# Kernel optimization log

Measured on AMD Instinct MI355X. Metric: run time of the kernel, lower is better.

## Reference

```python
import jax, jax.numpy as jnp
import numpy as np

NUM_EMBEDDINGS = 2048
EMBEDDING_DIM = 64
COMMITMENT_COST = 0.25


def setup_inputs() -> dict:
    key = jax.random.key(0)
    k1, k2 = jax.random.split(key)
    inputs = jax.random.normal(k1, (64, 32, 32, EMBEDDING_DIM), dtype=jnp.float32)
    # lecun_uniform-style scale on fan_in = embedding_dim
    limit = np.sqrt(3.0 / EMBEDDING_DIM).astype(np.float32)
    codebook = jax.random.uniform(k2, (EMBEDDING_DIM, NUM_EMBEDDINGS), dtype=jnp.float32,
                                  minval=-limit, maxval=limit)
    return {"inputs": inputs, "codebook": codebook}


def reference(inputs, codebook):
    lax = jax.lax
    flat = jnp.reshape(inputs, (-1, EMBEDDING_DIM))          # [N, D]
    # squared Euclidean distances to each code: [N, K]
    distances = (jnp.sum(jnp.square(flat), 1, keepdims=True)
                 - 2.0 * jnp.matmul(flat, codebook)
                 + jnp.sum(jnp.square(codebook), 0, keepdims=True))
    encoding_indices = jnp.argmin(distances, 1)              # [N]
    flat_q = jnp.take(codebook, encoding_indices, axis=1).swapaxes(1, 0)  # [N, D]
    quantized = jnp.reshape(flat_q, inputs.shape)

    codebook_loss = jnp.mean(jnp.square(quantized - lax.stop_gradient(inputs)))
    commitment_loss = COMMITMENT_COST * jnp.mean(
        jnp.square(lax.stop_gradient(quantized) - inputs))

    encodings = jax.nn.one_hot(encoding_indices, NUM_EMBEDDINGS, dtype=jnp.float32)
    avg_probs = jnp.mean(encodings, 0)
    perplexity = jnp.exp(-jnp.sum(avg_probs * jnp.log(avg_probs + 1e-10)))

    ste = inputs + lax.stop_gradient(quantized - inputs)
    return (ste, perplexity, codebook_loss, commitment_loss)
```

## Files before the change

### kernel.cpp

```cpp
#include <hip/hip_runtime.h>
#include <math.h>

#define KCODES 2048
#define DIM 64
#define NROWS 65536
#define NELEM (NROWS * DIM)

#define WS_HIST 0
#define WS_C2   8192
#define WS_C2S  16384
#define WS_SSE  24576
#define WS_P    32768

#define EPS_PK 33

typedef float  floatx4 __attribute__((ext_vector_type(4)));
typedef short  short8  __attribute__((ext_vector_type(8)));

__device__ __forceinline__ unsigned short f2bf(float f) {
  union { float f; unsigned u; } a; a.f = f;
  unsigned r = (a.u + 0x7FFFu + ((a.u >> 16) & 1u)) >> 16;
  return (unsigned short)r;
}
__device__ __forceinline__ float bf2f(unsigned short h) {
  union { unsigned u; float f; } a; a.u = ((unsigned)h) << 16;
  return a.f;
}

__global__ void vq_colnorm(const float* __restrict__ cb, float* __restrict__ c2,
                           float* __restrict__ c2s) {
  int k = blockIdx.x * 256 + threadIdx.x;
  float s = 0.f;
#pragma unroll
  for (int d = 0; d < DIM; ++d) {
    float v = cb[d * KCODES + k];
    s = fmaf(v, v, s);
  }
  c2[k] = s;
  c2s[k] = (s + 64.0f) * 16384.0f;
}

__global__ void vq_prep(const float* __restrict__ cb, char* __restrict__ P) {
  int tid = blockIdx.x * 256 + threadIdx.x;
  int code = tid & (KCODES - 1);
  int g = tid >> 11;
  short8 hh, ll;
#pragma unroll
  for (int e = 0; e < 8; ++e) {
    float v = -2.0f * cb[(size_t)(g * 8 + e) * KCODES + code];
    unsigned short hb = f2bf(v);
    float lo = v - bf2f(hb);
    hh[e] = (short)hb;
    ll[e] = (short)f2bf(lo);
  }
  int tile = code >> 5;
  int sn = code & 31;
  int pb = g ^ (sn & 7);
  size_t base = (size_t)tile * 8192 + sn * 128 + pb * 16;
  *(short8*)(P + base) = hh;
  *(short8*)(P + base + 4096) = ll;
}

__device__ __forceinline__ void stage_tile(const char* P, char* lds,
                                           int tile, int w, int lane) {
  const char* gp = P + (size_t)tile * 8192 + w * 1024 + lane * 16;
  char* lp = lds + w * 1024 + lane * 16;
  __builtin_amdgcn_global_load_lds(
      (const __attribute__((address_space(1))) unsigned*)gp,
      (__attribute__((address_space(3))) unsigned*)lp, 16, 0, 0);
  __builtin_amdgcn_global_load_lds(
      (const __attribute__((address_space(1))) unsigned*)(gp + 4096),
      (__attribute__((address_space(3))) unsigned*)(lp + 4096), 16, 0, 0);
}

__global__ __launch_bounds__(256, 2) void vq_main(
    const float* __restrict__ inp, const float* __restrict__ cb,
    const float* __restrict__ c2, const float* __restrict__ c2s,
    const char* __restrict__ P, int* __restrict__ hist,
    float* __restrict__ sse, float* __restrict__ out)
{
  __shared__ __align__(16) char Bstage[2][8192];
  __shared__ float s_c2s[KCODES];
  __shared__ int   s_k[128];
  __shared__ int   s_nflag;
  __shared__ int   s_frows[128];
  __shared__ float s_rd[256];
  __shared__ int   s_rk[256];
  __shared__ float s_red[4];

  const int t    = threadIdx.x;
  const int lane = t & 63;
  const int wave = __builtin_amdgcn_readfirstlane(t >> 6);
  const int c    = lane & 15;
  const int q    = lane >> 4;
  const int c7   = c & 7;
  const int rowbase = blockIdx.x * 128 + wave * 32;

  if (t == 0) s_nflag = 0;

#pragma unroll
  for (int i = 0; i < KCODES / 256; ++i) s_c2s[i * 256 + t] = c2s[i * 256 + t];

  short8 Ah[2][2], Al[2][2];
#pragma unroll
  for (int r = 0; r < 2; ++r) {
#pragma unroll
    for (int s = 0; s < 2; ++s) {
      const float* px = inp + (size_t)(rowbase + r * 16 + c) * 64 + s * 32 + q * 8;
      float4 u0 = *(const float4*)px;
      float4 u1 = *(const float4*)(px + 4);
      float u[8] = {u0.x, u0.y, u0.z, u0.w, u1.x, u1.y, u1.z, u1.w};
      short8 hh, ll;
#pragma unroll
      for (int e = 0; e < 8; ++e) {
        float xs = u[e] * 16384.0f;
        unsigned short hb = f2bf(xs);
        float lo = xs - bf2f(hb);
        hh[e] = (short)hb;
        ll[e] = (short)f2bf(lo);
      }
      Ah[r][s] = hh; Al[r][s] = ll;
    }
  }

  unsigned d1[8], d2[8];
#pragma unroll
  for (int i = 0; i < 8; ++i) { d1[i] = 0xFFFFFFFFu; d2[i] = 0xFFFFFFFFu; }

  stage_tile(P, Bstage[0], 0, wave, lane);
  __syncthreads();

  const floatx4 zero = {0.f, 0.f, 0.f, 0.f};

#pragma unroll 2
  for (int j = 0; j < 64; ++j) {
    const int buf = j & 1;
    if (j + 1 < 64) stage_tile(P, Bstage[1 - buf], j + 1, wave, lane);

    float c2v0 = s_c2s[j * 32 + c];
    float c2v1 = s_c2s[j * 32 + 16 + c];

#pragma unroll
    for (int nt = 0; nt < 2; ++nt) {
      const int rowi = nt * 16 + c;
      const char* bp = &Bstage[buf][rowi * 128];
      short8 bh0 = *(const short8*)(bp + ((0 + q) ^ c7) * 16);
      short8 bh1 = *(const short8*)(bp + ((4 + q) ^ c7) * 16);
      short8 bl0 = *(const short8*)(bp + 4096 + ((0 + q) ^ c7) * 16);
      short8 bl1 = *(const short8*)(bp + 4096 + ((4 + q) ^ c7) * 16);
      const float c2v = nt ? c2v1 : c2v0;
      const unsigned kcn = j * 32 + nt * 16 + c;
#pragma unroll
      for (int r = 0; r < 2; ++r) {
        floatx4 acc = __builtin_amdgcn_mfma_f32_16x16x32_bf16(Al[r][1], bh1, zero, 0, 0, 0);
        acc = __builtin_amdgcn_mfma_f32_16x16x32_bf16(Ah[r][1], bl1, acc, 0, 0, 0);
        acc = __builtin_amdgcn_mfma_f32_16x16x32_bf16(Al[r][0], bh0, acc, 0, 0, 0);
        acc = __builtin_amdgcn_mfma_f32_16x16x32_bf16(Ah[r][0], bl0, acc, 0, 0, 0);
        acc = __builtin_amdgcn_mfma_f32_16x16x32_bf16(Ah[r][1], bh1, acc, 0, 0, 0);
        acc = __builtin_amdgcn_mfma_f32_16x16x32_bf16(Ah[r][0], bh0, acc, 0, 0, 0);
#pragma unroll
        for (int reg = 0; reg < 4; ++reg) {
          float dds = acc[reg] + c2v;
          unsigned u = (((unsigned)dds) << 11) + kcn;
          const int i = r * 4 + reg;
          d2[i] = min(d2[i], max(d1[i], u));
          d1[i] = min(d1[i], u);
        }
      }
    }
    __syncthreads();
  }

#pragma unroll
  for (int i = 0; i < 8; ++i) {
    unsigned D1 = d1[i], D2 = d2[i];
#pragma unroll
    for (int off = 1; off < 16; off <<= 1) {
      unsigned o1 = (unsigned)__shfl_xor((int)D1, off, 64);
      unsigned o2 = (unsigned)__shfl_xor((int)D2, off, 64);
      D2 = min(min(D2, o2), max(D1, o1));
      D1 = min(D1, o1);
    }
    if (c == 0) {
      int lrow = wave * 32 + (i >> 2) * 16 + q * 4 + (i & 3);
      s_k[lrow] = (int)(D1 & 2047u);
      if ((int)((D2 >> 11) - (D1 >> 11)) < EPS_PK) {
        int idx = atomicAdd(&s_nflag, 1);
        s_frows[idx] = lrow;
      }
    }
  }
  __syncthreads();

  const int nf = s_nflag;
  for (int f = 0; f < nf; ++f) {
    const int lrow = s_frows[f];
    const float* xr = inp + (size_t)(blockIdx.x * 128 + lrow) * 64;
    float xs[64];
    float x2 = 0.f;
#pragma unroll
    for (int i = 0; i < 16; ++i) {
      float4 v = *(const float4*)(xr + i * 4);
      xs[4 * i + 0] = v.x; xs[4 * i + 1] = v.y; xs[4 * i + 2] = v.z; xs[4 * i + 3] = v.w;
      x2 = fmaf(v.x, v.x, x2); x2 = fmaf(v.y, v.y, x2);
      x2 = fmaf(v.z, v.z, x2); x2 = fmaf(v.w, v.w, x2);
    }
    float dot[8];
#pragma unroll
    for (int cc = 0; cc < 8; ++cc) dot[cc] = 0.f;
    const float* cp = cb + t * 8;
#pragma unroll 4
    for (int d = 0; d < 64; ++d) {
      float xd = xs[d];
#pragma unroll
      for (int cc = 0; cc < 8; ++cc)
        dot[cc] = fmaf(xd, cp[(size_t)d * KCODES + cc], dot[cc]);
    }
    float bd = INFINITY; int bk = 0;
#pragma unroll
    for (int cc = 0; cc < 8; ++cc) {
      float dd = (x2 - 2.0f * dot[cc]) + c2[t * 8 + cc];
      if (dd < bd) { bd = dd; bk = t * 8 + cc; }
    }
    s_rd[t] = bd; s_rk[t] = bk;
    __syncthreads();
    for (int s = 128; s >= 1; s >>= 1) {
      if (t < s) {
        if (s_rd[t + s] < s_rd[t]) { s_rd[t] = s_rd[t + s]; s_rk[t] = s_rk[t + s]; }
      }
      __syncthreads();
    }
    if (t == 0) s_k[lrow] = s_rk[0];
    __syncthreads();
  }

  if (t < 128) atomicAdd(&hist[s_k[t]], 1);

  const int fr = t >> 1;
  const int fd = (t & 1) * 32;
  const int grow = blockIdx.x * 128 + fr;
  const int myk = s_k[fr];
  const float* xrow = inp + (size_t)grow * 64 + fd;
  float* orow = out + (size_t)grow * 64 + fd;
  float serr = 0.f;
#pragma unroll
  for (int i = 0; i < 32; ++i) {
    float xv = xrow[i];
    float qv = cb[(size_t)(fd + i) * KCODES + myk];
    float dq = qv - xv;
    serr = fmaf(dq, dq, serr);
    orow[i] = xv + dq;
  }
#pragma unroll
  for (int off = 32; off > 0; off >>= 1) serr += __shfl_down(serr, off, 64);
  if (lane == 0) s_red[wave] = serr;
  __syncthreads();
  if (t == 0) atomicAdd(sse, s_red[0] + s_red[1] + s_red[2] + s_red[3]);
}

__global__ void vq_final(const int* __restrict__ hist,
                         const float* __restrict__ sse,
                         float* __restrict__ out) {
  __shared__ float s_red[4];
  const int t = threadIdx.x;
  float s = 0.f;
  for (int k = t; k < KCODES; k += 256) {
    float p = (float)hist[k] * (1.0f / NROWS);
    s += p * logf(p + 1e-10f);
  }
#pragma unroll
  for (int off = 32; off > 0; off >>= 1) s += __shfl_down(s, off, 64);
  if ((t & 63) == 0) s_red[t >> 6] = s;
  __syncthreads();
  if (t == 0) {
    float tot = s_red[0] + s_red[1] + s_red[2] + s_red[3];
    out[NELEM] = expf(-tot);
    float cl = *sse * (1.0f / NELEM);
    out[NELEM + 1] = cl;
    out[NELEM + 2] = 0.25f * cl;
  }
}

extern "C" void kernel_launch(void* const* d_in, const int* in_sizes, int n_in,
                              void* d_out, int out_size, void* d_ws, size_t ws_size,
                              hipStream_t stream) {
  const float* inp = (const float*)d_in[0];
  const float* cb  = (const float*)d_in[1];
  float* out = (float*)d_out;
  char* ws = (char*)d_ws;
  int*   hist = (int*)(ws + WS_HIST);
  float* c2   = (float*)(ws + WS_C2);
  float* c2s  = (float*)(ws + WS_C2S);
  float* sse  = (float*)(ws + WS_SSE);
  char*  P    = ws + WS_P;

  hipMemsetAsync(d_ws, 0, WS_SSE + 16, stream);
  vq_colnorm<<<KCODES / 256, 256, 0, stream>>>(cb, c2, c2s);
  vq_prep<<<KCODES * 8 / 256, 256, 0, stream>>>(cb, P);
  vq_main<<<NROWS / 128, 256, 0, stream>>>(inp, cb, c2, c2s, P, hist, sse, out);
  vq_final<<<1, 256, 0, stream>>>(hist, sse, out);
}
```

Before: 187.8 us.

## Restructure VQ kernel: register-resident codebook tiles, split codes across waves, fused launches

```diff
diff --git a/kernel.cpp b/kernel.cpp
--- a/kernel.cpp
+++ b/kernel.cpp
@@ -10,6 +10,7 @@
 #define WS_C2   8192
 #define WS_C2S  16384
 #define WS_SSE  24576
+#define WS_DONE 24580
 #define WS_P    32768
 
 #define EPS_PK 33
@@ -26,87 +27,77 @@
   union { unsigned u; float f; } a; a.u = ((unsigned)h) << 16;
   return a.f;
 }
-
-__global__ void vq_colnorm(const float* __restrict__ cb, float* __restrict__ c2,
-                           float* __restrict__ c2s) {
-  int k = blockIdx.x * 256 + threadIdx.x;
-  float s = 0.f;
-#pragma unroll
-  for (int d = 0; d < DIM; ++d) {
-    float v = cb[d * KCODES + k];
-    s = fmaf(v, v, s);
-  }
-  c2[k] = s;
-  c2s[k] = (s + 64.0f) * 16384.0f;
-}
-
-__global__ void vq_prep(const float* __restrict__ cb, char* __restrict__ P) {
-  int tid = blockIdx.x * 256 + threadIdx.x;
-  int code = tid & (KCODES - 1);
-  int g = tid >> 11;
-  short8 hh, ll;
+__device__ __forceinline__ unsigned umin2(unsigned a, unsigned b) { return a < b ? a : b; }
+__device__ __forceinline__ unsigned umax2(unsigned a, unsigned b) { return a > b ? a : b; }
+
+__global__ void vq_prep(const float* __restrict__ cb, char* __restrict__ P,
+                        float* __restrict__ c2, float* __restrict__ c2s,
+                        int* __restrict__ hist, float* __restrict__ sse,
+                        int* __restrict__ done) {
+  const int id = blockIdx.x * 256 + threadIdx.x;
+  const int c   = id & 15;
+  const int q   = (id >> 4) & 3;
+  const int s   = (id >> 6) & 1;
+  const int p   = (id >> 7) & 1;
+  const int t16 = id >> 8;
+  const int code = t16 * 16 + c;
+  const int d0 = s * 32 + q * 8;
+  short8 o;
 #pragma unroll
   for (int e = 0; e < 8; ++e) {
-    float v = -2.0f * cb[(size_t)(g * 8 + e) * KCODES + code];
+    float v = -2.0f * cb[(size_t)(d0 + e) * KCODES + code];
     unsigned short hb = f2bf(v);
     float lo = v - bf2f(hb);
-    hh[e] = (short)hb;
-    ll[e] = (short)f2bf(lo);
-  }
-  int tile = code >> 5;
-  int sn = code & 31;
-  int pb = g ^ (sn & 7);
-  size_t base = (size_t)tile * 8192 + sn * 128 + pb * 16;
-  *(short8*)(P + base) = hh;
-  *(short8*)(P + base + 4096) = ll;
-}
-
-__device__ __forceinline__ void stage_tile(const char* P, char* lds,
-                                           int tile, int w, int lane) {
-  const char* gp = P + (size_t)tile * 8192 + w * 1024 + lane * 16;
-  char* lp = lds + w * 1024 + lane * 16;
-  __builtin_amdgcn_global_load_lds(
-      (const __attribute__((address_space(1))) unsigned*)gp,
-      (__attribute__((address_space(3))) unsigned*)lp, 16, 0, 0);
-  __builtin_amdgcn_global_load_lds(
-      (const __attribute__((address_space(1))) unsigned*)(gp + 4096),
-      (__attribute__((address_space(3))) unsigned*)(lp + 4096), 16, 0, 0);
+    o[e] = p ? (short)f2bf(lo) : (short)hb;
+  }
+  *(short8*)(P + (size_t)id * 16) = o;
+
+  if (id < KCODES) {
+    float ss = 0.f;
+#pragma unroll
+    for (int d = 0; d < DIM; ++d) {
+      float v = cb[d * KCODES + id];
+      ss = fmaf(v, v, ss);
+    }
+    c2[id] = ss;
+    c2s[id] = (ss + 64.0f) * 16384.0f;
+    hist[id] = 0;
+    if (id == 0) { *sse = 0.f; *done = 0; }
+  }
 }
 
 __global__ __launch_bounds__(256, 2) void vq_main(
     const float* __restrict__ inp, const float* __restrict__ cb,
     const float* __restrict__ c2, const float* __restrict__ c2s,
     const char* __restrict__ P, int* __restrict__ hist,
-    float* __restrict__ sse, float* __restrict__ out)
+    float* __restrict__ sse, int* __restrict__ done, float* __restrict__ out)
 {
-  __shared__ __align__(16) char Bstage[2][8192];
-  __shared__ float s_c2s[KCODES];
+  __shared__ unsigned s_m1[2][128], s_m2[2][128];
   __shared__ int   s_k[128];
   __shared__ int   s_nflag;
   __shared__ int   s_frows[128];
   __shared__ float s_rd[256];
   __shared__ int   s_rk[256];
   __shared__ float s_red[4];
+  __shared__ int   s_last;
 
   const int t    = threadIdx.x;
   const int lane = t & 63;
   const int wave = __builtin_amdgcn_readfirstlane(t >> 6);
+  const int rg   = wave & 1;
+  const int ch   = wave >> 1;
   const int c    = lane & 15;
   const int q    = lane >> 4;
-  const int c7   = c & 7;
-  const int rowbase = blockIdx.x * 128 + wave * 32;
+  const int rowbase = blockIdx.x * 128 + rg * 64;
 
   if (t == 0) s_nflag = 0;
 
-#pragma unroll
-  for (int i = 0; i < KCODES / 256; ++i) s_c2s[i * 256 + t] = c2s[i * 256 + t];
-
-  short8 Ah[2][2], Al[2][2];
-#pragma unroll
-  for (int r = 0; r < 2; ++r) {
+  short8 Ah[4][2], Al[4][2];
+#pragma unroll
+  for (int rt = 0; rt < 4; ++rt) {
 #pragma unroll
     for (int s = 0; s < 2; ++s) {
-      const float* px = inp + (size_t)(rowbase + r * 16 + c) * 64 + s * 32 + q * 8;
+      const float* px = inp + (size_t)(rowbase + rt * 16 + c) * 64 + s * 32 + q * 8;
       float4 u0 = *(const float4*)px;
       float4 u1 = *(const float4*)(px + 4);
       float u[8] = {u0.x, u0.y, u0.z, u0.w, u1.x, u1.y, u1.z, u1.w};
@@ -119,75 +110,99 @@
         hh[e] = (short)hb;
         ll[e] = (short)f2bf(lo);
       }
-      Ah[r][s] = hh; Al[r][s] = ll;
-    }
-  }
-
-  unsigned d1[8], d2[8];
-#pragma unroll
-  for (int i = 0; i < 8; ++i) { d1[i] = 0xFFFFFFFFu; d2[i] = 0xFFFFFFFFu; }
-
-  stage_tile(P, Bstage[0], 0, wave, lane);
-  __syncthreads();
-
-  const floatx4 zero = {0.f, 0.f, 0.f, 0.f};
-
-#pragma unroll 2
-  for (int j = 0; j < 64; ++j) {
-    const int buf = j & 1;
-    if (j + 1 < 64) stage_tile(P, Bstage[1 - buf], j + 1, wave, lane);
-
-    float c2v0 = s_c2s[j * 32 + c];
-    float c2v1 = s_c2s[j * 32 + 16 + c];
-
+      Ah[rt][s] = hh; Al[rt][s] = ll;
+    }
+  }
+
+  unsigned d1[16], d2[16];
+#pragma unroll
+  for (int i = 0; i < 16; ++i) { d1[i] = 0xFFFFFFFFu; d2[i] = 0xFFFFFFFFu; }
+
+  const char* Pw = P + ((size_t)ch << 18);
+  const float* c2sw = c2s + ch * 1024;
+
+  auto load_tile = [&](short8 B[2][4], int j) {
+#pragma unroll
+    for (int nt = 0; nt < 2; ++nt)
+#pragma unroll
+      for (int f = 0; f < 4; ++f)
+        B[nt][f] = *(const short8*)(Pw + ((((j * 2 + nt) * 4 + f) << 10) + lane * 16));
+  };
+
+  auto comp_tile = [&](short8 B[2][4], int j) {
 #pragma unroll
     for (int nt = 0; nt < 2; ++nt) {
-      const int rowi = nt * 16 + c;
-      const char* bp = &Bstage[buf][rowi * 128];
-      short8 bh0 = *(const short8*)(bp + ((0 + q) ^ c7) * 16);
-      short8 bh1 = *(const short8*)(bp + ((4 + q) ^ c7) * 16);
-      short8 bl0 = *(const short8*)(bp + 4096 + ((0 + q) ^ c7) * 16);
-      short8 bl1 = *(const short8*)(bp + 4096 + ((4 + q) ^ c7) * 16);
-      const float c2v = nt ? c2v1 : c2v0;
-      const unsigned kcn = j * 32 + nt * 16 + c;
-#pragma unroll
-      for (int r = 0; r < 2; ++r) {
-        floatx4 acc = __builtin_amdgcn_mfma_f32_16x16x32_bf16(Al[r][1], bh1, zero, 0, 0, 0);
-        acc = __builtin_amdgcn_mfma_f32_16x16x32_bf16(Ah[r][1], bl1, acc, 0, 0, 0);
-        acc = __builtin_amdgcn_mfma_f32_16x16x32_bf16(Al[r][0], bh0, acc, 0, 0, 0);
-        acc = __builtin_amdgcn_mfma_f32_16x16x32_bf16(Ah[r][0], bl0, acc, 0, 0, 0);
-        acc = __builtin_amdgcn_mfma_f32_16x16x32_bf16(Ah[r][1], bh1, acc, 0, 0, 0);
-        acc = __builtin_amdgcn_mfma_f32_16x16x32_bf16(Ah[r][0], bh0, acc, 0, 0, 0);
+      float c2v = c2sw[j * 32 + nt * 16 + c];
+      floatx4 ci = {c2v, c2v, c2v, c2v};
+      floatx4 acc[4];
+#pragma unroll
+      for (int rt = 0; rt < 4; ++rt)
+        acc[rt] = __builtin_amdgcn_mfma_f32_16x16x32_bf16(Al[rt][1], B[nt][1], ci, 0, 0, 0);
+#pragma unroll
+      for (int rt = 0; rt < 4; ++rt)
+        acc[rt] = __builtin_amdgcn_mfma_f32_16x16x32_bf16(Ah[rt][1], B[nt][3], acc[rt], 0, 0, 0);
+#pragma unroll
+      for (int rt = 0; rt < 4; ++rt)
+        acc[rt] = __builtin_amdgcn_mfma_f32_16x16x32_bf16(Al[rt][0], B[nt][0], acc[rt], 0, 0, 0);
+#pragma unroll
+      for (int rt = 0; rt < 4; ++rt)
+        acc[rt] = __builtin_amdgcn_mfma_f32_16x16x32_bf16(Ah[rt][0], B[nt][2], acc[rt], 0, 0, 0);
+#pragma unroll
+      for (int rt = 0; rt < 4; ++rt)
+        acc[rt] = __builtin_amdgcn_mfma_f32_16x16x32_bf16(Ah[rt][1], B[nt][1], acc[rt], 0, 0, 0);
+#pragma unroll
+      for (int rt = 0; rt < 4; ++rt)
+        acc[rt] = __builtin_amdgcn_mfma_f32_16x16x32_bf16(Ah[rt][0], B[nt][0], acc[rt], 0, 0, 0);
+      const unsigned kcn = ch * 1024 + j * 32 + nt * 16 + c;
+#pragma unroll
+      for (int rt = 0; rt < 4; ++rt)
 #pragma unroll
         for (int reg = 0; reg < 4; ++reg) {
-          float dds = acc[reg] + c2v;
-          unsigned u = (((unsigned)dds) << 11) + kcn;
-          const int i = r * 4 + reg;
-          d2[i] = min(d2[i], max(d1[i], u));
-          d1[i] = min(d1[i], u);
+          unsigned u = (((unsigned)acc[rt][reg]) << 11) + kcn;
+          const int i = rt * 4 + reg;
+          d2[i] = umin2(d2[i], umax2(d1[i], u));
+          d1[i] = umin2(d1[i], u);
         }
-      }
-    }
-    __syncthreads();
-  }
-
-#pragma unroll
-  for (int i = 0; i < 8; ++i) {
+    }
+  };
+
+  short8 BA[2][4], BB[2][4];
+  load_tile(BA, 0);
+#pragma unroll 1
+  for (int j = 0; j < 32; j += 2) {
+    load_tile(BB, j + 1);
+    comp_tile(BA, j);
+    if (j + 2 < 32) load_tile(BA, j + 2);
+    comp_tile(BB, j + 1);
+  }
+
+#pragma unroll
+  for (int i = 0; i < 16; ++i) {
     unsigned D1 = d1[i], D2 = d2[i];
 #pragma unroll
     for (int off = 1; off < 16; off <<= 1) {
       unsigned o1 = (unsigned)__shfl_xor((int)D1, off, 64);
       unsigned o2 = (unsigned)__shfl_xor((int)D2, off, 64);
-      D2 = min(min(D2, o2), max(D1, o1));
-      D1 = min(D1, o1);
+      D2 = umin2(umin2(D2, o2), umax2(D1, o1));
+      D1 = umin2(D1, o1);
     }
     if (c == 0) {
-      int lrow = wave * 32 + (i >> 2) * 16 + q * 4 + (i & 3);
-      s_k[lrow] = (int)(D1 & 2047u);
-      if ((int)((D2 >> 11) - (D1 >> 11)) < EPS_PK) {
-        int idx = atomicAdd(&s_nflag, 1);
-        s_frows[idx] = lrow;
-      }
+      int lr = rg * 64 + (i >> 2) * 16 + q * 4 + (i & 3);
+      s_m1[ch][lr] = D1;
+      s_m2[ch][lr] = D2;
+    }
+  }
+  __syncthreads();
+
+  if (t < 128) {
+    unsigned a1 = s_m1[0][t], a2 = s_m2[0][t];
+    unsigned b1 = s_m1[1][t], b2 = s_m2[1][t];
+    unsigned D1 = umin2(a1, b1);
+    unsigned D2 = umin2(umin2(a2, b2), umax2(a1, b1));
+    s_k[t] = (int)(D1 & 2047u);
+    if ((int)((D2 >> 11) - (D1 >> 11)) < EPS_PK) {
+      int idx = atomicAdd(&s_nflag, 1);
+      s_frows[idx] = t;
     }
   }
   __syncthreads();
@@ -256,28 +271,28 @@
   if (lane == 0) s_red[wave] = serr;
   __syncthreads();
   if (t == 0) atomicAdd(sse, s_red[0] + s_red[1] + s_red[2] + s_red[3]);
-}
-
-__global__ void vq_final(const int* __restrict__ hist,
-                         const float* __restrict__ sse,
-                         float* __restrict__ out) {
-  __shared__ float s_red[4];
-  const int t = threadIdx.x;
-  float s = 0.f;
-  for (int k = t; k < KCODES; k += 256) {
-    float p = (float)hist[k] * (1.0f / NROWS);
-    s += p * logf(p + 1e-10f);
-  }
-#pragma unroll
-  for (int off = 32; off > 0; off >>= 1) s += __shfl_down(s, off, 64);
-  if ((t & 63) == 0) s_red[t >> 6] = s;
+
+  __threadfence();
+  if (t == 0) s_last = (atomicAdd(done, 1) == (int)gridDim.x - 1);
   __syncthreads();
-  if (t == 0) {
-    float tot = s_red[0] + s_red[1] + s_red[2] + s_red[3];
-    out[NELEM] = expf(-tot);
-    float cl = *sse * (1.0f / NELEM);
-    out[NELEM + 1] = cl;
-    out[NELEM + 2] = 0.25f * cl;
+  if (s_last) {
+    float s = 0.f;
+    for (int k = t; k < KCODES; k += 256) {
+      int h = atomicAdd(&hist[k], 0);
+      float pp = (float)h * (1.0f / NROWS);
+      s += pp * logf(pp + 1e-10f);
+    }
+#pragma unroll
+    for (int off = 32; off > 0; off >>= 1) s += __shfl_down(s, off, 64);
+    if (lane == 0) s_red[wave] = s;
+    __syncthreads();
+    if (t == 0) {
+      float tot = s_red[0] + s_red[1] + s_red[2] + s_red[3];
+      out[NELEM] = expf(-tot);
+      float cl = atomicAdd(sse, 0.0f) * (1.0f / NELEM);
+      out[NELEM + 1] = cl;
+      out[NELEM + 2] = 0.25f * cl;
+    }
   }
 }
 
@@ -292,11 +307,9 @@
   float* c2   = (float*)(ws + WS_C2);
   float* c2s  = (float*)(ws + WS_C2S);
   float* sse  = (float*)(ws + WS_SSE);
+  int*   done = (int*)(ws + WS_DONE);
   char*  P    = ws + WS_P;
 
-  hipMemsetAsync(d_ws, 0, WS_SSE + 16, stream);
-  vq_colnorm<<<KCODES / 256, 256, 0, stream>>>(cb, c2, c2s);
-  vq_prep<<<KCODES * 8 / 256, 256, 0, stream>>>(cb, P);
-  vq_main<<<NROWS / 128, 256, 0, stream>>>(inp, cb, c2, c2s, P, hist, sse, out);
-  vq_final<<<1, 256, 0, stream>>>(hist, sse, out);
-}
+  vq_prep<<<128, 256, 0, stream>>>(cb, P, c2, c2s, hist, sse, done);
+  vq_main<<<NROWS / 128, 256, 0, stream>>>(inp, cb, c2, c2s, P, hist, sse, done, out);
+}
```

Result: slower. 248.2 us (+32.2%).
